# Kernel tuning notes

Measured on AMD Instinct MI355X. Metric: run time of the kernel, lower is better.

The kernel has to match this reference:

```python
import jax, jax.numpy as jnp
import numpy as np

N_NODES = 10000
N_EDGES = 160000
IN_DIM, HID_DIM, OUT_DIM = 256, 512, 256


def gcn_conv(x, W, b, src, dst, dinv):
    # PyG GCNConv with add_self_loops=True and symmetric normalization.
    # dinv = deg^{-1/2} computed once (degrees include self loops).
    h = x @ W                                   # [N, F_out]
    norm = dinv[src] * dinv[dst]                # [E]
    msg = h[src] * norm[:, None]                # gather + scale, [E, F_out]
    agg = jnp.zeros_like(h).at[dst].add(msg)    # scatter-add over edges
    agg = agg + h * (dinv * dinv)[:, None]      # self-loop contribution
    return agg + b


def setup_inputs() -> dict:
    key = jax.random.key(0)
    ks = jax.random.split(key, 8)
    x = jax.random.normal(ks[0], (N_NODES, IN_DIM), dtype=jnp.float32)
    edge_index = jax.random.randint(ks[1], (2, N_EDGES), 0, N_NODES, dtype=jnp.int64)

    def glorot(k, fan_in, fan_out):
        s = jnp.sqrt(6.0 / (fan_in + fan_out)).astype(jnp.float32)
        return jax.random.uniform(k, (fan_in, fan_out), jnp.float32, -s, s)

    return {
        "x": x,
        "W1": glorot(ks[2], IN_DIM, HID_DIM), "b1": jnp.zeros((HID_DIM,), jnp.float32),
        "W2": glorot(ks[3], HID_DIM, HID_DIM), "b2": jnp.zeros((HID_DIM,), jnp.float32),
        "W3": glorot(ks[4], HID_DIM, OUT_DIM), "b3": jnp.zeros((OUT_DIM,), jnp.float32),
        "edge_index": edge_index,
    }


def reference(x, W1, b1, W2, b2, W3, b3, edge_index):
    src, dst = edge_index[0], edge_index[1]
    n = x.shape[0]
    # degree with self loops (edge weight 1), shared by all three layers
    deg = jnp.zeros((n,), x.dtype).at[dst].add(1.0) + 1.0
    dinv = jax.lax.rsqrt(deg)
    h = jnp.tanh(gcn_conv(x, W1, b1, src, dst, dinv))
    h = jnp.tanh(gcn_conv(h, W2, b2, src, dst, dinv))
    out = gcn_conv(h, W3, b3, src, dst, dinv)
    return out
```

## Files before the change

### kernel.cpp

```cpp
#include <hip/hip_runtime.h>
#include <math.h>

#define NN 10000
#define NE 160000
#define IN_DIM 256
#define HID_DIM 512
#define OUT_DIM 256

typedef unsigned short u16;
typedef _Float16 f16x8 __attribute__((ext_vector_type(8)));
typedef __attribute__((ext_vector_type(4))) float f32x4;


union F16U { _Float16 h; u16 u; };
static __device__ __forceinline__ u16 f2h_bits(float f) {
    F16U v; v.h = (_Float16)f; return v.u;
}


__global__ void k_init(const float* __restrict__ W1, const float* __restrict__ W2,
                       const float* __restrict__ W3, const float* __restrict__ x,
                       u16* __restrict__ W1h, u16* __restrict__ W1l,
                       u16* __restrict__ W2h, u16* __restrict__ W2l,
                       u16* __restrict__ W3h, u16* __restrict__ W3l,
                       u16* __restrict__ xh, int* __restrict__ deg) {
    int idx = blockIdx.x * blockDim.x + threadIdx.x;
    const int S1 = IN_DIM * HID_DIM;
    const int S2 = HID_DIM * HID_DIM;
    const int S3 = HID_DIM * OUT_DIM;
    const int TW = S1 + S2 + S3;
    const int TX = NN * IN_DIM;
    if (idx < TW) {
        const float* W; u16 *Th, *Tl; int K, N, local;
        if (idx < S1)           { W = W1; Th = W1h; Tl = W1l; K = IN_DIM;  N = HID_DIM; local = idx; }
        else if (idx < S1 + S2) { W = W2; Th = W2h; Tl = W2l; K = HID_DIM; N = HID_DIM; local = idx - S1; }
        else                    { W = W3; Th = W3h; Tl = W3l; K = HID_DIM; N = OUT_DIM; local = idx - S1 - S2; }
        int k = local / N, n = local - k * N;
        float v = W[local];
        F16U hh; hh.h = (_Float16)v;
        float r = (v - (float)hh.h) * 2048.0f;
        Th[(size_t)n * K + k] = hh.u;
        Tl[(size_t)n * K + k] = f2h_bits(r);
    } else if (idx < TW + TX) {
        int j = idx - TW;
        xh[j] = f2h_bits(x[j]);
    } else if (idx < TW + TX + NN) {
        deg[idx - TW - TX] = 0;
    }
}


__global__ void k_count_deg(const int* __restrict__ dst, int* __restrict__ deg) {
    int e = blockIdx.x * blockDim.x + threadIdx.x;
    if (e < NE) atomicAdd(&deg[dst[e]], 1);
}

__launch_bounds__(1024)
__global__ void k_scan(const int* __restrict__ deg, int* __restrict__ row,
                       int* __restrict__ csr, float* __restrict__ dinv) {
    __shared__ int sdeg[10240];
    __shared__ int sums[1024];
    const int tid = threadIdx.x;
    for (int i = tid; i < NN; i += 1024) sdeg[i] = deg[i];
    __syncthreads();
    const int CH = 10;
    int base = tid * CH;
    int s = 0;
    for (int j = 0; j < CH; ++j) {
        int i = base + j;
        if (i < NN) s += sdeg[i] + 1;
    }
    sums[tid] = s;
    __syncthreads();
    for (int off = 1; off < 1024; off <<= 1) {
        int t = (tid >= off) ? sums[tid - off] : 0;
        __syncthreads();
        sums[tid] += t;
        __syncthreads();
    }
    int run = sums[tid] - s;
    for (int j = 0; j < CH; ++j) {
        int i = base + j;
        if (i < NN) {
            int dg = sdeg[i];
            csr[run] = i;
            row[i] = run + 1;
            dinv[i] = rsqrtf((float)dg + 1.0f);
            run += dg + 1;
        }
    }
}

__global__ void k_fill(const int* __restrict__ src, const int* __restrict__ dst,
                       int* __restrict__ row, int* __restrict__ csr) {
    int e = blockIdx.x * blockDim.x + threadIdx.x;
    if (e < NE) {
        int pos = atomicAdd(&row[dst[e]], 1);
        csr[pos] = src[e];
    }
}


struct PfSet { uint4 a0, a1, bh, bl; };

template<int K, bool HAS_BIAS, bool DO_TANH, bool F16_OUT, bool ROWSCALE>
__launch_bounds__(256)
__global__ void k_gemm_f16x2(const u16* __restrict__ A, const u16* __restrict__ Bhi,
                             const u16* __restrict__ Blo,
                             const float* __restrict__ bias, const float* __restrict__ rowscale,
                             float* __restrict__ C, u16* __restrict__ Ch,
                             int M, int N, int MT, int MT8) {
    __shared__ uint4 As[2][512];
    __shared__ uint4 BsH[2][256];
    __shared__ uint4 BsL[2][256];

    const int id = blockIdx.x;
    const int xcd = id & 7;
    const int q2 = id >> 3;
    const int mt = (q2 % MT8) * 8 + xcd;
    const int nt = q2 / MT8;
    if (mt >= MT) return;

    const int tid  = threadIdx.x;
    const int wave = tid >> 6;
    const int lane = tid & 63;
    const int lr   = lane & 15;
    const int quad = lane >> 4;
    const int m_base = mt * 128;
    const int n_base = nt * 64;

    const int s_row = tid >> 2;
    const int s_kq  = tid & 3;
    const int c_lo  = ((s_row >> 4) << 6) + s_kq * 16 + (s_row & 15);

    const u16* pA0 = A   + (size_t)(m_base + s_row) * K + s_kq * 8;
    const u16* pA1 = pA0 + (size_t)64 * K;
    const u16* pBh = Bhi + (size_t)(n_base + s_row) * K + s_kq * 8;
    const u16* pBl = Blo + (size_t)(n_base + s_row) * K + s_kq * 8;
    const bool g0 = (m_base + s_row) < M;
    const bool g1 = (m_base + s_row + 64) < M;

    const uint4 z = make_uint4(0u, 0u, 0u, 0u);

    auto load_set = [&](int it, PfSet& r) {
        const int ko = it * 32;
        r.a0 = z; r.a1 = z;
        if (g0) r.a0 = *(const uint4*)(pA0 + ko);
        if (g1) r.a1 = *(const uint4*)(pA1 + ko);
        r.bh = *(const uint4*)(pBh + ko);
        r.bl = *(const uint4*)(pBl + ko);
    };
    auto lds_write = [&](int buf, const PfSet& r) {
        As[buf][c_lo] = r.a0;
        As[buf][c_lo + 256] = r.a1;
        BsH[buf][c_lo] = r.bh;
        BsL[buf][c_lo] = r.bl;
    };

    f32x4 accH[2][4] = {};
    f32x4 accL[2][4] = {};

    auto compute = [&](int buf) {
        f16x8 a[2], bH[4], bL[4];
#pragma unroll
        for (int tm = 0; tm < 2; ++tm) {
            int c = (wave * 2 + tm) * 64 + lane;
            a[tm] = *(const f16x8*)&As[buf][c];
        }
#pragma unroll
        for (int tn = 0; tn < 4; ++tn) {
            int c = tn * 64 + lane;
            bH[tn] = *(const f16x8*)&BsH[buf][c];
            bL[tn] = *(const f16x8*)&BsL[buf][c];
        }
#pragma unroll
        for (int tm = 0; tm < 2; ++tm)
#pragma unroll
            for (int tn = 0; tn < 4; ++tn) {
                accH[tm][tn] = __builtin_amdgcn_mfma_f32_16x16x32_f16(a[tm], bH[tn], accH[tm][tn], 0, 0, 0);
                accL[tm][tn] = __builtin_amdgcn_mfma_f32_16x16x32_f16(a[tm], bL[tn], accL[tm][tn], 0, 0, 0);
            }
    };

    const int NIT = K >> 5;
    PfSet sA;

    load_set(0, sA);
    lds_write(0, sA);
    __syncthreads();

    for (int it = 0; it < NIT; ++it) {
        const bool has_next = (it + 1) < NIT;
        PfSet sN;
        if (has_next) load_set(it + 1, sN);
        compute(it & 1);
        if (has_next) lds_write((it + 1) & 1, sN);
        __syncthreads();
    }

#pragma unroll
    for (int tm = 0; tm < 2; ++tm) {
        int row0 = m_base + wave * 32 + tm * 16 + quad * 4;
#pragma unroll
        for (int i = 0; i < 4; ++i) {
            int row = row0 + i;
            if (row >= M) continue;
            float rs = ROWSCALE ? rowscale[row] : 1.0f;
#pragma unroll
            for (int tn = 0; tn < 4; ++tn) {
                int col = n_base + tn * 16 + lr;
                float v = accH[tm][tn][i] + accL[tm][tn][i] * (1.0f / 2048.0f);
                if (HAS_BIAS) v += bias[col];
                if (DO_TANH) v = tanhf(v);
                if (ROWSCALE) v *= rs;
                if (F16_OUT) {
                    Ch[(size_t)row * N + col] = f2h_bits(v);
                } else {
                    C[(size_t)row * N + col] = v;
                }
            }
        }
    }
}


template<bool PRESCALED, bool HAS_BIAS, bool F16_OUT, int F>
__launch_bounds__(256)
__global__ void k_gather_h(const u16* __restrict__ h, const float* __restrict__ dinv,
                           const int* __restrict__ row_end, const int* __restrict__ csr,
                           const float* __restrict__ bias,
                           float* __restrict__ outF, u16* __restrict__ outH) {
    constexpr int L  = F / 8;
    constexpr int LS = L / 8;
    constexpr int NPB = 256 / LS;
    const int tid = threadIdx.x;
    const int d = (blockIdx.x >> 3) * NPB + tid / LS;
    if (d >= NN) return;
    const int f8 = (blockIdx.x & 7) * LS + (tid & (LS - 1));

    const int start = (d == 0) ? 0 : row_end[d - 1];
    const int end = row_end[d];
    const uint4* h16 = (const uint4*)h;

    float acc[8] = {};
    int e = start;
    for (; e + 8 <= end; e += 8) {
        int s[8]; uint4 raw[8]; float w[8];
#pragma unroll
        for (int j = 0; j < 8; ++j) s[j] = csr[e + j];
#pragma unroll
        for (int j = 0; j < 8; ++j) raw[j] = h16[(size_t)s[j] * L + f8];
#pragma unroll
        for (int j = 0; j < 8; ++j) w[j] = PRESCALED ? 1.0f : dinv[s[j]];
#pragma unroll
        for (int j = 0; j < 8; ++j) {
            f16x8 hv = *(const f16x8*)&raw[j];
#pragma unroll
            for (int t = 0; t < 8; ++t) acc[t] += w[j] * (float)hv[t];
        }
    }
    for (; e < end; ++e) {
        int s = csr[e];
        float w = PRESCALED ? 1.0f : dinv[s];
        uint4 raw = h16[(size_t)s * L + f8];
        f16x8 hv = *(const f16x8*)&raw;
#pragma unroll
        for (int t = 0; t < 8; ++t) acc[t] += w * (float)hv[t];
    }

    const float dd = dinv[d];
    float r[8];
#pragma unroll
    for (int t = 0; t < 8; ++t) r[t] = dd * acc[t];
    if (HAS_BIAS) {
        const float4* b4 = (const float4*)bias;
        float4 b0 = b4[f8 * 2], b1 = b4[f8 * 2 + 1];
        r[0] += b0.x; r[1] += b0.y; r[2] += b0.z; r[3] += b0.w;
        r[4] += b1.x; r[5] += b1.y; r[6] += b1.z; r[7] += b1.w;
    }
    if (F16_OUT) {
        union { u16 a[8]; uint4 v; } pk;
#pragma unroll
        for (int t = 0; t < 8; ++t) pk.a[t] = f2h_bits(r[t]);
        ((uint4*)outH)[(size_t)d * L + f8] = pk.v;
    } else {
        size_t base = (size_t)d * (F / 4) + f8 * 2;
        ((float4*)outF)[base]     = make_float4(r[0], r[1], r[2], r[3]);
        ((float4*)outF)[base + 1] = make_float4(r[4], r[5], r[6], r[7]);
    }
}


extern "C" void kernel_launch(void* const* d_in, const int* in_sizes, int n_in,
                              void* d_out, int out_size, void* d_ws, size_t ws_size,
                              hipStream_t stream) {
    const float* x  = (const float*)d_in[0];
    const float* W1 = (const float*)d_in[1];
    const float* b1 = (const float*)d_in[2];
    const float* W2 = (const float*)d_in[3];
    const float* b2 = (const float*)d_in[4];
    const float* W3 = (const float*)d_in[5];
    const float* b3 = (const float*)d_in[6];
    const int* edge = (const int*)d_in[7];
    const int* src = edge;
    const int* dst = edge + NE;
    float* out = (float*)d_out;

    const size_t SLOT = (size_t)NN * HID_DIM * 4;
    char* p = (char*)d_ws;
    char* slot0 = p;
    char* slot1 = p + SLOT;
    char* q = p + 2 * SLOT;
    u16* W1Th = (u16*)q; q += (size_t)IN_DIM  * HID_DIM * 2;
    u16* W1Tl = (u16*)q; q += (size_t)IN_DIM  * HID_DIM * 2;
    u16* W2Th = (u16*)q; q += (size_t)HID_DIM * HID_DIM * 2;
    u16* W2Tl = (u16*)q; q += (size_t)HID_DIM * HID_DIM * 2;
    u16* W3Th = (u16*)q; q += (size_t)HID_DIM * OUT_DIM * 2;
    u16* W3Tl = (u16*)q; q += (size_t)HID_DIM * OUT_DIM * 2;
    int*   deg  = (int*)q;   q += (size_t)NN * 4;
    float* dinv = (float*)q; q += (size_t)NN * 4;
    int*   row  = (int*)q;   q += (size_t)NN * 4;
    int*   csr  = (int*)q;   q += (size_t)(NE + NN) * 4;
    u16*   xh   = (u16*)q;   q += (size_t)NN * IN_DIM * 2;

    u16* Xagg  = (u16*)slot0;
    u16* g1h   = (u16*)slot1;
    u16* H1agg = (u16*)slot0;
    u16* h2    = (u16*)slot1;
    u16* g3h   = (u16*)slot0;

    const int T = 256;
    const int MT = (NN + 127) / 128;
    const int MT8 = (MT + 7) / 8;

    {
        int total = IN_DIM * HID_DIM + HID_DIM * HID_DIM + HID_DIM * OUT_DIM
                  + NN * IN_DIM + NN;
        k_init<<<(total + T - 1) / T, T, 0, stream>>>(W1, W2, W3, x, W1Th, W1Tl,
                                                      W2Th, W2Tl, W3Th, W3Tl, xh, deg);
    }
    k_count_deg<<<(NE + T - 1) / T, T, 0, stream>>>(dst, deg);
    k_scan<<<1, 1024, 0, stream>>>(deg, row, csr, dinv);
    k_fill<<<(NE + T - 1) / T, T, 0, stream>>>(src, dst, row, csr);

    const int G256 = ((NN + 63) / 64) * 8;
    const int G512 = ((NN + 31) / 32) * 8;
    const int GEMM_G512 = 8 * MT8 * (HID_DIM / 64);
    const int GEMM_G256 = 8 * MT8 * (OUT_DIM / 64);

    k_gather_h<false, false, true, IN_DIM><<<G256, 256, 0, stream>>>(
        xh, dinv, row, csr, nullptr, nullptr, Xagg);
    k_gemm_f16x2<IN_DIM, true, true, true, true><<<GEMM_G512, 256, 0, stream>>>(
        Xagg, W1Th, W1Tl, b1, dinv, nullptr, g1h, NN, HID_DIM, MT, MT8);

    k_gather_h<true, false, true, HID_DIM><<<G512, 256, 0, stream>>>(
        g1h, dinv, row, csr, nullptr, nullptr, H1agg);
    k_gemm_f16x2<HID_DIM, true, true, true, false><<<GEMM_G512, 256, 0, stream>>>(
        H1agg, W2Th, W2Tl, b2, nullptr, nullptr, h2, NN, HID_DIM, MT, MT8);

    k_gemm_f16x2<HID_DIM, false, false, true, true><<<GEMM_G256, 256, 0, stream>>>(
        h2, W3Th, W3Tl, nullptr, dinv, nullptr, g3h, NN, OUT_DIM, MT, MT8);
    k_gather_h<true, true, false, OUT_DIM><<<G256, 256, 0, stream>>>(
        g3h, dinv, row, csr, b3, out, nullptr);

    (void)in_sizes; (void)n_in; (void)out_size; (void)ws_size;
}
```

Measured before the change: 226.2 us.

## Sort gather rows by degree, fold degree count into init, use 2-wave GEMM

Three changes at once. The degree counting is folded into the init kernel, with a memset in place of in-kernel zeroing, which removes one launch. The scan kernel now builds a degree-bucketed permutation that the gather kernels use, so threads handling nodes of similar degree sit together and load imbalance inside waves drops. The GEMM switches to 128 threads, where each wave computes 64 rows via a 4x4 MFMA tile. That doubles per-wave register use for accumulators and may lower occupancy, though the launch bound requests 2 blocks per CU.

New measurement: 243.7 us. 1.08x slower.

```diff
diff --git a/kernel.cpp b/kernel.cpp
--- a/kernel.cpp
+++ b/kernel.cpp
@@ -20,6 +20,7 @@
 
 __global__ void k_init(const float* __restrict__ W1, const float* __restrict__ W2,
                        const float* __restrict__ W3, const float* __restrict__ x,
+                       const int* __restrict__ dst,
                        u16* __restrict__ W1h, u16* __restrict__ W1l,
                        u16* __restrict__ W2h, u16* __restrict__ W2l,
                        u16* __restrict__ W3h, u16* __restrict__ W3l,
@@ -44,23 +45,22 @@
     } else if (idx < TW + TX) {
         int j = idx - TW;
         xh[j] = f2h_bits(x[j]);
-    } else if (idx < TW + TX + NN) {
-        deg[idx - TW - TX] = 0;
-    }
-}
-
-
-__global__ void k_count_deg(const int* __restrict__ dst, int* __restrict__ deg) {
-    int e = blockIdx.x * blockDim.x + threadIdx.x;
-    if (e < NE) atomicAdd(&deg[dst[e]], 1);
-}
+    } else if (idx < TW + TX + NE) {
+        atomicAdd(&deg[dst[idx - TW - TX]], 1);
+    }
+}
+
 
 __launch_bounds__(1024)
 __global__ void k_scan(const int* __restrict__ deg, int* __restrict__ row,
-                       int* __restrict__ csr, float* __restrict__ dinv) {
+                       int* __restrict__ csr, float* __restrict__ dinv,
+                       int* __restrict__ perm) {
     __shared__ int sdeg[10240];
     __shared__ int sums[1024];
+    __shared__ int hist[64];
+    __shared__ int hoff[64];
     const int tid = threadIdx.x;
+    if (tid < 64) hist[tid] = 0;
     for (int i = tid; i < NN; i += 1024) sdeg[i] = deg[i];
     __syncthreads();
     const int CH = 10;
@@ -68,7 +68,11 @@
     int s = 0;
     for (int j = 0; j < CH; ++j) {
         int i = base + j;
-        if (i < NN) s += sdeg[i] + 1;
+        if (i < NN) {
+            int dg = sdeg[i];
+            s += dg + 1;
+            atomicAdd(&hist[dg < 63 ? dg : 63], 1);
+        }
     }
     sums[tid] = s;
     __syncthreads();
@@ -78,6 +82,13 @@
         sums[tid] += t;
         __syncthreads();
     }
+    if (tid == 0) {
+        int acc = 0;
+        for (int b = 0; b < 64; ++b) { hoff[b] = acc; acc += hist[b]; }
+    }
+    __syncthreads();
+    if (tid < 64) hist[tid] = hoff[tid];
+    __syncthreads();
     int run = sums[tid] - s;
     for (int j = 0; j < CH; ++j) {
         int i = base + j;
@@ -87,6 +98,8 @@
             row[i] = run + 1;
             dinv[i] = rsqrtf((float)dg + 1.0f);
             run += dg + 1;
+            int pos = atomicAdd(&hist[dg < 63 ? dg : 63], 1);
+            perm[pos] = i;
         }
     }
 }
@@ -101,10 +114,10 @@
 }
 
 
-struct PfSet { uint4 a0, a1, bh, bl; };
+struct PfSet { uint4 a[4], bh[2], bl[2]; };
 
 template<int K, bool HAS_BIAS, bool DO_TANH, bool F16_OUT, bool ROWSCALE>
-__launch_bounds__(256)
+__launch_bounds__(128, 2)
 __global__ void k_gemm_f16x2(const u16* __restrict__ A, const u16* __restrict__ Bhi,
                              const u16* __restrict__ Blo,
                              const float* __restrict__ bias, const float* __restrict__ rowscale,
@@ -131,55 +144,59 @@
 
     const int s_row = tid >> 2;
     const int s_kq  = tid & 3;
-    const int c_lo  = ((s_row >> 4) << 6) + s_kq * 16 + (s_row & 15);
+    const int c0    = ((s_row >> 4) << 6) + s_kq * 16 + (s_row & 15);
 
     const u16* pA0 = A   + (size_t)(m_base + s_row) * K + s_kq * 8;
-    const u16* pA1 = pA0 + (size_t)64 * K;
     const u16* pBh = Bhi + (size_t)(n_base + s_row) * K + s_kq * 8;
     const u16* pBl = Blo + (size_t)(n_base + s_row) * K + s_kq * 8;
-    const bool g0 = (m_base + s_row) < M;
-    const bool g1 = (m_base + s_row + 64) < M;
+    bool g[4];
+#pragma unroll
+    for (int j = 0; j < 4; ++j) g[j] = (m_base + s_row + j * 32) < M;
 
     const uint4 z = make_uint4(0u, 0u, 0u, 0u);
 
     auto load_set = [&](int it, PfSet& r) {
         const int ko = it * 32;
-        r.a0 = z; r.a1 = z;
-        if (g0) r.a0 = *(const uint4*)(pA0 + ko);
-        if (g1) r.a1 = *(const uint4*)(pA1 + ko);
-        r.bh = *(const uint4*)(pBh + ko);
-        r.bl = *(const uint4*)(pBl + ko);
+#pragma unroll
+        for (int j = 0; j < 4; ++j) {
+            r.a[j] = z;
+            if (g[j]) r.a[j] = *(const uint4*)(pA0 + (size_t)j * 32 * K + ko);
+        }
+#pragma unroll
+        for (int j = 0; j < 2; ++j) {
+            r.bh[j] = *(const uint4*)(pBh + (size_t)j * 32 * K + ko);
+            r.bl[j] = *(const uint4*)(pBl + (size_t)j * 32 * K + ko);
+        }
     };
     auto lds_write = [&](int buf, const PfSet& r) {
-        As[buf][c_lo] = r.a0;
-        As[buf][c_lo + 256] = r.a1;
-        BsH[buf][c_lo] = r.bh;
-        BsL[buf][c_lo] = r.bl;
+#pragma unroll
+        for (int j = 0; j < 4; ++j) As[buf][c0 + j * 128] = r.a[j];
+#pragma unroll
+        for (int j = 0; j < 2; ++j) {
+            BsH[buf][c0 + j * 128] = r.bh[j];
+            BsL[buf][c0 + j * 128] = r.bl[j];
+        }
     };
 
-    f32x4 accH[2][4] = {};
-    f32x4 accL[2][4] = {};
+    f32x4 accH[4][4] = {};
+    f32x4 accL[4][4] = {};
 
     auto compute = [&](int buf) {
-        f16x8 a[2], bH[4], bL[4];
-#pragma unroll
-        for (int tm = 0; tm < 2; ++tm) {
-            int c = (wave * 2 + tm) * 64 + lane;
-            a[tm] = *(const f16x8*)&As[buf][c];
-        }
+        f16x8 bH[4], bL[4];
 #pragma unroll
         for (int tn = 0; tn < 4; ++tn) {
-            int c = tn * 64 + lane;
-            bH[tn] = *(const f16x8*)&BsH[buf][c];
-            bL[tn] = *(const f16x8*)&BsL[buf][c];
-        }
-#pragma unroll
-        for (int tm = 0; tm < 2; ++tm)
+            bH[tn] = *(const f16x8*)&BsH[buf][tn * 64 + lane];
+            bL[tn] = *(const f16x8*)&BsL[buf][tn * 64 + lane];
+        }
+#pragma unroll
+        for (int tm = 0; tm < 4; ++tm) {
+            f16x8 a = *(const f16x8*)&As[buf][(wave * 4 + tm) * 64 + lane];
 #pragma unroll
             for (int tn = 0; tn < 4; ++tn) {
-                accH[tm][tn] = __builtin_amdgcn_mfma_f32_16x16x32_f16(a[tm], bH[tn], accH[tm][tn], 0, 0, 0);
-                accL[tm][tn] = __builtin_amdgcn_mfma_f32_16x16x32_f16(a[tm], bL[tn], accL[tm][tn], 0, 0, 0);
+                accH[tm][tn] = __builtin_amdgcn_mfma_f32_16x16x32_f16(a, bH[tn], accH[tm][tn], 0, 0, 0);
+                accL[tm][tn] = __builtin_amdgcn_mfma_f32_16x16x32_f16(a, bL[tn], accL[tm][tn], 0, 0, 0);
             }
+        }
     };
 
     const int NIT = K >> 5;
@@ -199,8 +216,8 @@
     }
 
 #pragma unroll
-    for (int tm = 0; tm < 2; ++tm) {
-        int row0 = m_base + wave * 32 + tm * 16 + quad * 4;
+    for (int tm = 0; tm < 4; ++tm) {
+        int row0 = m_base + wave * 64 + tm * 16 + quad * 4;
 #pragma unroll
         for (int i = 0; i < 4; ++i) {
             int row = row0 + i;
@@ -228,14 +245,15 @@
 __launch_bounds__(256)
 __global__ void k_gather_h(const u16* __restrict__ h, const float* __restrict__ dinv,
                            const int* __restrict__ row_end, const int* __restrict__ csr,
-                           const float* __restrict__ bias,
+                           const int* __restrict__ perm, const float* __restrict__ bias,
                            float* __restrict__ outF, u16* __restrict__ outH) {
     constexpr int L  = F / 8;
     constexpr int LS = L / 8;
     constexpr int NPB = 256 / LS;
     const int tid = threadIdx.x;
-    const int d = (blockIdx.x >> 3) * NPB + tid / LS;
-    if (d >= NN) return;
+    const int widx = (blockIdx.x >> 3) * NPB + tid / LS;
+    if (widx >= NN) return;
+    const int d = perm[widx];
     const int f8 = (blockIdx.x & 7) * LS + (tid & (LS - 1));
 
     const int start = (d == 0) ? 0 : row_end[d - 1];
@@ -320,6 +338,7 @@
     int*   deg  = (int*)q;   q += (size_t)NN * 4;
     float* dinv = (float*)q; q += (size_t)NN * 4;
     int*   row  = (int*)q;   q += (size_t)NN * 4;
+    int*   perm = (int*)q;   q += (size_t)NN * 4;
     int*   csr  = (int*)q;   q += (size_t)(NE + NN) * 4;
     u16*   xh   = (u16*)q;   q += (size_t)NN * IN_DIM * 2;
 
@@ -333,14 +352,14 @@
     const int MT = (NN + 127) / 128;
     const int MT8 = (MT + 7) / 8;
 
+    hipMemsetAsync(deg, 0, (size_t)NN * 4, stream);
     {
         int total = IN_DIM * HID_DIM + HID_DIM * HID_DIM + HID_DIM * OUT_DIM
-                  + NN * IN_DIM + NN;
-        k_init<<<(total + T - 1) / T, T, 0, stream>>>(W1, W2, W3, x, W1Th, W1Tl,
+                  + NN * IN_DIM + NE;
+        k_init<<<(total + T - 1) / T, T, 0, stream>>>(W1, W2, W3, x, dst, W1Th, W1Tl,
                                                       W2Th, W2Tl, W3Th, W3Tl, xh, deg);
     }
-    k_count_deg<<<(NE + T - 1) / T, T, 0, stream>>>(dst, deg);
-    k_scan<<<1, 1024, 0, stream>>>(deg, row, csr, dinv);
+    k_scan<<<1, 1024, 0, stream>>>(deg, row, csr, dinv, perm);
     k_fill<<<(NE + T - 1) / T, T, 0, stream>>>(src, dst, row, csr);
 
     const int G256 = ((NN + 63) / 64) * 8;
@@ -349,19 +368,19 @@
     const int GEMM_G256 = 8 * MT8 * (OUT_DIM / 64);
 
     k_gather_h<false, false, true, IN_DIM><<<G256, 256, 0, stream>>>(
-        xh, dinv, row, csr, nullptr, nullptr, Xagg);
-    k_gemm_f16x2<IN_DIM, true, true, true, true><<<GEMM_G512, 256, 0, stream>>>(
+        xh, dinv, row, csr, perm, nullptr, nullptr, Xagg);
+    k_gemm_f16x2<IN_DIM, true, true, true, true><<<GEMM_G512, 128, 0, stream>>>(
         Xagg, W1Th, W1Tl, b1, dinv, nullptr, g1h, NN, HID_DIM, MT, MT8);
 
     k_gather_h<true, false, true, HID_DIM><<<G512, 256, 0, stream>>>(
-        g1h, dinv, row, csr, nullptr, nullptr, H1agg);
-    k_gemm_f16x2<HID_DIM, true, true, true, false><<<GEMM_G512, 256, 0, stream>>>(
+        g1h, dinv, row, csr, perm, nullptr, nullptr, H1agg);
+    k_gemm_f16x2<HID_DIM, true, true, true, false><<<GEMM_G512, 128, 0, stream>>>(
         H1agg, W2Th, W2Tl, b2, nullptr, nullptr, h2, NN, HID_DIM, MT, MT8);
 
-    k_gemm_f16x2<HID_DIM, false, false, true, true><<<GEMM_G256, 256, 0, stream>>>(
+    k_gemm_f16x2<HID_DIM, false, false, true, true><<<GEMM_G256, 128, 0, stream>>>(
         h2, W3Th, W3Tl, nullptr, dinv, nullptr, g3h, NN, OUT_DIM, MT, MT8);
     k_gather_h<true, true, false, OUT_DIM><<<G256, 256, 0, stream>>>(
-        g3h, dinv, row, csr, b3, out, nullptr);
+        g3h, dinv, row, csr, perm, b3, out, nullptr);
 
     (void)in_sizes; (void)n_in; (void)out_size; (void)ws_size;
 }
```
